# Performance work log

Hardware: AMD Instinct MI355X
Metric: run time of the kernel (lower is better)

The kernel has to match this reference:

```python
import jax, jax.numpy as jnp
import numpy as np

N = 4096
K = 3          # from loss_name 'LMNN-3'
MU = 0.5       # default mu in LMNN
NUM_CLASSES = 10


def setup_inputs() -> dict:
    key = jax.random.key(0)
    k1, k2 = jax.random.split(key)
    distances_sq = jax.random.uniform(k1, (N, N), dtype=jnp.float32)
    labels = jax.random.randint(k2, (N, 1), 0, NUM_CLASSES, dtype=jnp.int32)
    return {"distances_sq": distances_sq, "labels": labels}


def lmnn(D, labels, k=K, mu=MU):
    n = D.shape[0]
    same = (labels == labels.T).astype(D.dtype)              # [n,n] same-class indicator
    cross = same * (1.0 - jnp.eye(n, dtype=D.dtype))         # exclude self-pairs
    order = jnp.argsort(D, axis=-1)                          # ascending per row
    pull_mask = jnp.take_along_axis(cross, order, axis=-1)[:, : k + 1]   # [n,k+1]
    sortD = jnp.take_along_axis(D, order, axis=-1)[:, : k + 1]           # [n,k+1]
    pull_d = sortD * pull_mask                               # masked k+1 nearest distances
    pull = jnp.sum(pull_d)
    # push: sum_{i,m,j} relu((pull_d[i,m] - D[j,i] + 1) * pull_mask[i,m] * (1 - same[j,i]))
    # vectorized form of the original per-row Python loop; hinge is [n, k+1, n]
    hinge = jax.nn.relu(
        (pull_d[:, :, None] - D.T[:, None, :] + 1.0)
        * pull_mask[:, :, None]
        * (1.0 - same.T)[:, None, :]
    )
    push = jnp.sum(hinge)
    return (1.0 - mu) * pull + mu * push


def reference(distances_sq, labels):
    # grad_reverse is identity in the forward pass
    return lmnn(distances_sq, labels)
```

## Files before the change

kernel.cpp:

```cpp
#include <hip/hip_runtime.h>

#define N 4096
#define NCLS 10
#define RPB 4
#define NBLK (N / RPB)
#define CRG 16
#define CRC (NBLK / CRG)
#define CAP 160
#define THRESH 0.015625f

__device__ __forceinline__ bool lessvi(float v1, int i1, float v2, int i2) {
    return (v1 < v2) || (v1 == v2 && i1 < i2);
}

__device__ __forceinline__ void insert4(float vv, int ci, float tv[4], int ti[4]) {
    if (lessvi(vv, ci, tv[3], ti[3])) {
        tv[3] = vv; ti[3] = ci;
#pragma unroll
        for (int q2 = 3; q2 > 0; --q2) {
            const bool sw = lessvi(tv[q2], ti[q2], tv[q2 - 1], ti[q2 - 1]);
            const float av = tv[q2 - 1]; const int ai = ti[q2 - 1];
            tv[q2 - 1] = sw ? tv[q2] : av;
            ti[q2 - 1] = sw ? ti[q2] : ai;
            tv[q2]     = sw ? av : tv[q2];
            ti[q2]     = sw ? ai : ti[q2];
        }
    }
}

__global__ __launch_bounds__(256) void stream_pass(const float* __restrict__ D,
                                                   const int* __restrict__ labels,
                                                   float* __restrict__ pdiff,
                                                   float* __restrict__ cand_v,
                                                   int* __restrict__ cand_i,
                                                   int* __restrict__ cand_cnt) {
    __shared__ int scnt[RPB];
    const int tid = threadIdx.x;
    const int r0  = blockIdx.x * RPB;
    if (tid < RPB) scnt[tid] = 0;
    __syncthreads();

    int4 cl[4];
#pragma unroll
    for (int q = 0; q < 4; ++q) cl[q] = ((const int4*)labels)[tid + 256 * q];

    float4 diff[4] = {{0,0,0,0},{0,0,0,0},{0,0,0,0},{0,0,0,0}};

    const float4* rp = (const float4*)(D + (size_t)r0 * N);
    float4 vc[4], vn[4];
#pragma unroll
    for (int q = 0; q < 4; ++q) vc[q] = rp[tid + 256 * q];

#pragma unroll
    for (int r = 0; r < RPB; ++r) {
        if (r < RPB - 1) {
            const float4* np = rp + (size_t)(r + 1) * (N / 4);
#pragma unroll
            for (int q = 0; q < 4; ++q) vn[q] = np[tid + 256 * q];
        }
        const int row    = r0 + r;
        const int rowlab = labels[row];
#pragma unroll
        for (int q = 0; q < 4; ++q) {
            const float4 v = vc[q];
            diff[q].x += (cl[q].x != rowlab) ? v.x : 0.f;
            diff[q].y += (cl[q].y != rowlab) ? v.y : 0.f;
            diff[q].z += (cl[q].z != rowlab) ? v.z : 0.f;
            diff[q].w += (cl[q].w != rowlab) ? v.w : 0.f;

            const int c0 = 4 * tid + 1024 * q;
            const float vals[4] = {v.x, v.y, v.z, v.w};
#pragma unroll
            for (int e = 0; e < 4; ++e) {
                if (vals[e] < THRESH) {
                    const int idx = atomicAdd(&scnt[r], 1);
                    if (idx < CAP) {
                        cand_v[(size_t)row * CAP + idx] = vals[e];
                        cand_i[(size_t)row * CAP + idx] = c0 + e;
                    }
                }
            }
        }
#pragma unroll
        for (int q = 0; q < 4; ++q) vc[q] = vn[q];
    }

    float4* op = (float4*)(pdiff + (size_t)blockIdx.x * N);
#pragma unroll
    for (int q = 0; q < 4; ++q) op[tid + 256 * q] = diff[q];

    __syncthreads();
    if (tid < RPB) cand_cnt[r0 + tid] = scnt[tid];
}

__global__ __launch_bounds__(256) void select_top4(const float* __restrict__ D,
                                                   const int* __restrict__ labels,
                                                   const float* __restrict__ cand_v,
                                                   const int* __restrict__ cand_i,
                                                   const int* __restrict__ cand_cnt,
                                                   float* __restrict__ pd_sum,
                                                   float* __restrict__ a_cnt) {
    const int lane = threadIdx.x & 63;
    const int wave = threadIdx.x >> 6;
    const int row  = blockIdx.x * 4 + wave;
    const int cnt  = cand_cnt[row];

    float tv[4] = {INFINITY, INFINITY, INFINITY, INFINITY};
    int   ti[4] = {0x7ffffff0, 0x7ffffff1, 0x7ffffff2, 0x7ffffff3};

    if (cnt >= 4 && cnt <= CAP) {
        for (int k = lane; k < cnt; k += 64)
            insert4(cand_v[(size_t)row * CAP + k], cand_i[(size_t)row * CAP + k], tv, ti);
    } else {
        const float4* rp4 = (const float4*)(D + (size_t)row * N);
        for (int s = 0; s < 16; ++s) {
            const float4 q = rp4[s * 64 + lane];
            const int c0 = (s * 64 + lane) * 4;
            insert4(q.x, c0, tv, ti);
            insert4(q.y, c0 + 1, tv, ti);
            insert4(q.z, c0 + 2, tv, ti);
            insert4(q.w, c0 + 3, tv, ti);
        }
    }

#pragma unroll
    for (int off = 1; off < 64; off <<= 1) {
        float yv[4]; int yi[4];
#pragma unroll
        for (int k = 0; k < 4; ++k) {
            yv[k] = __shfl_xor(tv[k], off);
            yi[k] = __shfl_xor(ti[k], off);
        }
        float rv[4]; int ri[4];
#pragma unroll
        for (int k = 0; k < 4; ++k) {
            const bool tm = lessvi(tv[0], ti[0], yv[0], yi[0]);
            rv[k] = tm ? tv[0] : yv[0];
            ri[k] = tm ? ti[0] : yi[0];
#pragma unroll
            for (int q2 = 0; q2 < 3; ++q2) {
                tv[q2] = tm ? tv[q2 + 1] : tv[q2];
                ti[q2] = tm ? ti[q2 + 1] : ti[q2];
                yv[q2] = tm ? yv[q2]     : yv[q2 + 1];
                yi[q2] = tm ? yi[q2]     : yi[q2 + 1];
            }
        }
#pragma unroll
        for (int k = 0; k < 4; ++k) { tv[k] = rv[k]; ti[k] = ri[k]; }
    }

    if (lane == 0) {
        const int li = labels[row];
        float pd = 0.f, a = 0.f;
#pragma unroll
        for (int m = 0; m < 4; ++m) {
            const int j = ti[m];
            if (j != row && labels[j] == li) { pd += tv[m]; a += 1.f; }
        }
        pd_sum[row] = pd;
        a_cnt[row]  = a;
    }
}

__global__ __launch_bounds__(256) void col_reduce(const float* __restrict__ pdiff,
                                                  float* __restrict__ cdiff) {
    const int tile = blockIdx.x & 3;
    const int g    = blockIdx.x >> 2;
    const int col  = tile * 1024 + threadIdx.x * 4;
    float4 acc = {0.f, 0.f, 0.f, 0.f};
#pragma unroll 8
    for (int ch = 0; ch < CRC; ++ch) {
        const float4 v = *(const float4*)(pdiff + (size_t)(g * CRC + ch) * N + col);
        acc.x += v.x; acc.y += v.y; acc.z += v.z; acc.w += v.w;
    }
    *(float4*)(cdiff + (size_t)g * N + col) = acc;
}

__global__ __launch_bounds__(256) void finalize(const int* __restrict__ labels,
                                                const float* __restrict__ pd_sum,
                                                const float* __restrict__ a_cnt,
                                                const float* __restrict__ cdiff,
                                                float* __restrict__ out) {
    __shared__ int    cnt[NCLS];
    __shared__ double red[256];
    const int tid = threadIdx.x;

    if (tid < NCLS) cnt[tid] = 0;
    __syncthreads();
    for (int i = tid; i < N; i += 256) atomicAdd(&cnt[labels[i]], 1);
    __syncthreads();

    double acc = 0.0;
    for (int i = tid; i < N; i += 256) {
        const int li = labels[i];
        const double pd = (double)pd_sum[i];
        const double a  = (double)a_cnt[i];
        float csf = 0.f;
#pragma unroll
        for (int g = 0; g < CRG; ++g) csf += cdiff[(size_t)g * N + i];
        const double cs = (double)csf;
        const double cd = (double)(N - cnt[li]);
        acc += pd;
        acc += cd * (pd + a) - a * cs;
    }
    red[tid] = acc;
    __syncthreads();
    for (int s = 128; s > 0; s >>= 1) {
        if (tid < s) red[tid] += red[tid + s];
        __syncthreads();
    }
    if (tid == 0) out[0] = (float)(0.5 * red[0]);
}

extern "C" void kernel_launch(void* const* d_in, const int* in_sizes, int n_in,
                              void* d_out, int out_size, void* d_ws, size_t ws_size,
                              hipStream_t stream) {
    const float* D      = (const float*)d_in[0];
    const int*   labels = (const int*)d_in[1];
    float*       out    = (float*)d_out;

    float* pdiff    = (float*)d_ws;
    float* cdiff    = pdiff + (size_t)NBLK * N;
    float* pd_sum   = cdiff + (size_t)CRG * N;
    float* a_cnt    = pd_sum + N;
    float* cand_v   = a_cnt + N;
    int*   cand_i   = (int*)(cand_v + (size_t)N * CAP);
    int*   cand_cnt = cand_i + (size_t)N * CAP;

    stream_pass<<<NBLK, 256, 0, stream>>>(D, labels, pdiff, cand_v, cand_i, cand_cnt);
    select_top4<<<N / 4, 256, 0, stream>>>(D, labels, cand_v, cand_i, cand_cnt, pd_sum, a_cnt);
    col_reduce<<<CRG * 4, 256, 0, stream>>>(pdiff, cdiff);
    finalize<<<1, 256, 0, stream>>>(labels, pd_sum, a_cnt, cdiff, out);
}
```

Measured before the change: 122.5 us.

## Tile streaming pass in 2D: 16-row chunks by 4 column slices

The streaming kernel now assigns each block 16 rows and one 1024-column slice instead of 4 full rows, so each thread holds one float4 per row rather than four. This cuts the partial-sum buffer from 1024 to 256 rows per column, which shrinks the column-reduce workload. Candidate lists are split per slice with their own counts and capacity, and the top-4 selector merges the four slices. Fewer registers per thread and less partial-sum traffic are traded for less load parallelism per thread and a longer serial loop per block.

```diff
diff --git a/kernel.cpp b/kernel.cpp
--- a/kernel.cpp
+++ b/kernel.cpp
@@ -2,12 +2,13 @@
 
 #define N 4096
 #define NCLS 10
-#define RPB 4
-#define NBLK (N / RPB)
-#define CRG 16
-#define CRC (NBLK / CRG)
-#define CAP 160
+#define RPB 16
+#define NCHUNK (N / RPB)
+#define NSLICE 4
+#define CAPS 64
 #define THRESH 0.015625f
+#define CRG 8
+#define CRC (NCHUNK / CRG)
 
 __device__ __forceinline__ bool lessvi(float v1, int i1, float v2, int i2) {
     return (v1 < v2) || (v1 == v2 && i1 < i2);
@@ -28,69 +29,59 @@
     }
 }
 
-__global__ __launch_bounds__(256) void stream_pass(const float* __restrict__ D,
-                                                   const int* __restrict__ labels,
-                                                   float* __restrict__ pdiff,
-                                                   float* __restrict__ cand_v,
-                                                   int* __restrict__ cand_i,
-                                                   int* __restrict__ cand_cnt) {
+__global__ __launch_bounds__(256) void stream2d(const float* __restrict__ D,
+                                                const int* __restrict__ labels,
+                                                float* __restrict__ pdiff,
+                                                float* __restrict__ cand_v,
+                                                int* __restrict__ cand_i,
+                                                int* __restrict__ cand_cnt) {
     __shared__ int scnt[RPB];
-    const int tid = threadIdx.x;
-    const int r0  = blockIdx.x * RPB;
+    const int tid   = threadIdx.x;
+    const int slice = blockIdx.x & 3;
+    const int chunk = blockIdx.x >> 2;
+    const int r0    = chunk * RPB;
+    const int c0    = slice * 1024 + tid * 4;
+
     if (tid < RPB) scnt[tid] = 0;
     __syncthreads();
 
-    int4 cl[4];
-#pragma unroll
-    for (int q = 0; q < 4; ++q) cl[q] = ((const int4*)labels)[tid + 256 * q];
-
-    float4 diff[4] = {{0,0,0,0},{0,0,0,0},{0,0,0,0},{0,0,0,0}};
-
-    const float4* rp = (const float4*)(D + (size_t)r0 * N);
-    float4 vc[4], vn[4];
-#pragma unroll
-    for (int q = 0; q < 4; ++q) vc[q] = rp[tid + 256 * q];
+    const int4 cl = *(const int4*)(labels + c0);
+    float4 diff = {0.f, 0.f, 0.f, 0.f};
+
+    const float* rowbase = D + (size_t)r0 * N + slice * 1024;
+    float4 vc = ((const float4*)rowbase)[tid];
 
 #pragma unroll
     for (int r = 0; r < RPB; ++r) {
-        if (r < RPB - 1) {
-            const float4* np = rp + (size_t)(r + 1) * (N / 4);
-#pragma unroll
-            for (int q = 0; q < 4; ++q) vn[q] = np[tid + 256 * q];
-        }
+        float4 vn;
+        if (r < RPB - 1) vn = ((const float4*)(rowbase + (size_t)(r + 1) * N))[tid];
         const int row    = r0 + r;
         const int rowlab = labels[row];
-#pragma unroll
-        for (int q = 0; q < 4; ++q) {
-            const float4 v = vc[q];
-            diff[q].x += (cl[q].x != rowlab) ? v.x : 0.f;
-            diff[q].y += (cl[q].y != rowlab) ? v.y : 0.f;
-            diff[q].z += (cl[q].z != rowlab) ? v.z : 0.f;
-            diff[q].w += (cl[q].w != rowlab) ? v.w : 0.f;
-
-            const int c0 = 4 * tid + 1024 * q;
-            const float vals[4] = {v.x, v.y, v.z, v.w};
-#pragma unroll
-            for (int e = 0; e < 4; ++e) {
-                if (vals[e] < THRESH) {
-                    const int idx = atomicAdd(&scnt[r], 1);
-                    if (idx < CAP) {
-                        cand_v[(size_t)row * CAP + idx] = vals[e];
-                        cand_i[(size_t)row * CAP + idx] = c0 + e;
-                    }
+
+        diff.x += (cl.x != rowlab) ? vc.x : 0.f;
+        diff.y += (cl.y != rowlab) ? vc.y : 0.f;
+        diff.z += (cl.z != rowlab) ? vc.z : 0.f;
+        diff.w += (cl.w != rowlab) ? vc.w : 0.f;
+
+        const float vals[4] = {vc.x, vc.y, vc.z, vc.w};
+#pragma unroll
+        for (int e = 0; e < 4; ++e) {
+            if (vals[e] < THRESH) {
+                const int idx = atomicAdd(&scnt[r], 1);
+                if (idx < CAPS) {
+                    const size_t slot = (size_t)row * (NSLICE * CAPS) + slice * CAPS + idx;
+                    cand_v[slot] = vals[e];
+                    cand_i[slot] = c0 + e;
                 }
             }
         }
-#pragma unroll
-        for (int q = 0; q < 4; ++q) vc[q] = vn[q];
-    }
-
-    float4* op = (float4*)(pdiff + (size_t)blockIdx.x * N);
-#pragma unroll
-    for (int q = 0; q < 4; ++q) op[tid + 256 * q] = diff[q];
-
-    __syncthreads();
-    if (tid < RPB) cand_cnt[r0 + tid] = scnt[tid];
+        vc = vn;
+    }
+
+    *(float4*)(pdiff + (size_t)chunk * N + c0) = diff;
+
+    __syncthreads();
+    if (tid < RPB) cand_cnt[(size_t)(r0 + tid) * NSLICE + slice] = scnt[tid];
 }
 
 __global__ __launch_bounds__(256) void select_top4(const float* __restrict__ D,
@@ -103,23 +94,32 @@
     const int lane = threadIdx.x & 63;
     const int wave = threadIdx.x >> 6;
     const int row  = blockIdx.x * 4 + wave;
-    const int cnt  = cand_cnt[row];
+
+    const int4 cnt4 = *(const int4*)(cand_cnt + (size_t)row * NSLICE);
+    const int cs[4] = {cnt4.x, cnt4.y, cnt4.z, cnt4.w};
+    const int total = cs[0] + cs[1] + cs[2] + cs[3];
+    const bool ok = (total >= 4) && (cs[0] <= CAPS) && (cs[1] <= CAPS) &&
+                    (cs[2] <= CAPS) && (cs[3] <= CAPS);
 
     float tv[4] = {INFINITY, INFINITY, INFINITY, INFINITY};
     int   ti[4] = {0x7ffffff0, 0x7ffffff1, 0x7ffffff2, 0x7ffffff3};
 
-    if (cnt >= 4 && cnt <= CAP) {
-        for (int k = lane; k < cnt; k += 64)
-            insert4(cand_v[(size_t)row * CAP + k], cand_i[(size_t)row * CAP + k], tv, ti);
+    if (ok) {
+#pragma unroll
+        for (int s = 0; s < 4; ++s) {
+            const size_t base = (size_t)row * (NSLICE * CAPS) + s * CAPS;
+            for (int k = lane; k < cs[s]; k += 64)
+                insert4(cand_v[base + k], cand_i[base + k], tv, ti);
+        }
     } else {
         const float4* rp4 = (const float4*)(D + (size_t)row * N);
         for (int s = 0; s < 16; ++s) {
             const float4 q = rp4[s * 64 + lane];
-            const int c0 = (s * 64 + lane) * 4;
-            insert4(q.x, c0, tv, ti);
-            insert4(q.y, c0 + 1, tv, ti);
-            insert4(q.z, c0 + 2, tv, ti);
-            insert4(q.w, c0 + 3, tv, ti);
+            const int cc = (s * 64 + lane) * 4;
+            insert4(q.x, cc, tv, ti);
+            insert4(q.y, cc + 1, tv, ti);
+            insert4(q.z, cc + 2, tv, ti);
+            insert4(q.w, cc + 3, tv, ti);
         }
     }
 
@@ -220,14 +220,14 @@
     float*       out    = (float*)d_out;
 
     float* pdiff    = (float*)d_ws;
-    float* cdiff    = pdiff + (size_t)NBLK * N;
+    float* cdiff    = pdiff + (size_t)NCHUNK * N;
     float* pd_sum   = cdiff + (size_t)CRG * N;
     float* a_cnt    = pd_sum + N;
     float* cand_v   = a_cnt + N;
-    int*   cand_i   = (int*)(cand_v + (size_t)N * CAP);
-    int*   cand_cnt = cand_i + (size_t)N * CAP;
-
-    stream_pass<<<NBLK, 256, 0, stream>>>(D, labels, pdiff, cand_v, cand_i, cand_cnt);
+    int*   cand_i   = (int*)(cand_v + (size_t)N * NSLICE * CAPS);
+    int*   cand_cnt = cand_i + (size_t)N * NSLICE * CAPS;
+
+    stream2d<<<NCHUNK * NSLICE, 256, 0, stream>>>(D, labels, pdiff, cand_v, cand_i, cand_cnt);
     select_top4<<<N / 4, 256, 0, stream>>>(D, labels, cand_v, cand_i, cand_cnt, pd_sum, a_cnt);
     col_reduce<<<CRG * 4, 256, 0, stream>>>(pdiff, cdiff);
     finalize<<<1, 256, 0, stream>>>(labels, pd_sum, a_cnt, cdiff, out);
```

Result: no change. 121.6 us (-0.8%).
